# Performance work log

Measured on AMD Instinct MI355X. Metric: run time of the kernel, lower is better.

## Reference

```python
import jax, jax.numpy as jnp
import numpy as np

IN_DIM = 512
HID = 1024
E = 16
TOPK = 2


def setup_inputs() -> dict:
    key = jax.random.key(0)
    ks = jax.random.split(key, 8)
    s = 0.02
    x = jax.random.normal(ks[0], (4, 2048, IN_DIM), dtype=jnp.float32)
    Wr = jax.random.normal(ks[1], (IN_DIM, E), dtype=jnp.float32) * s
    br = jnp.zeros((E,), dtype=jnp.float32)
    W1 = jax.random.normal(ks[2], (E, IN_DIM, HID), dtype=jnp.float32) * s
    b1 = jnp.zeros((E, HID), dtype=jnp.float32)
    W2 = jax.random.normal(ks[3], (E, HID, IN_DIM), dtype=jnp.float32) * s
    b2 = jnp.zeros((E, IN_DIM), dtype=jnp.float32)
    return {"x": x, "Wr": Wr, "br": br, "W1": W1, "b1": b1, "W2": W2, "b2": b2}


def reference(x, Wr, br, W1, b1, W2, b2):
    token_shape = x.shape[:-1]
    xf = x.reshape(-1, x.shape[-1])            # [T, D]
    T = xf.shape[0]

    # router (temperature = 1.0)
    logits = xf @ Wr + br                       # [T, E]
    probs = jax.nn.softmax(logits, axis=-1)
    topk_w, topk_idx = jax.lax.top_k(probs, TOPK)           # [T, K]
    topk_w = topk_w / jnp.maximum(topk_w.sum(-1, keepdims=True), 1e-9)

    # combine weights: [T, E], zero where not routed
    combine = jnp.zeros((T, E), dtype=xf.dtype).at[
        jnp.arange(T)[:, None], topk_idx].add(topk_w)

    # per-expert MLP (exact GELU, as torch nn.GELU default), weighted combine
    y = jnp.zeros_like(xf)
    for e in range(E):
        h = jax.nn.gelu(xf @ W1[e] + b1[e], approximate=False)  # [T, H]
        o = h @ W2[e] + b2[e]                                   # [T, D]
        y = y + combine[:, e:e + 1] * o

    # residual (in_dim == out_dim)
    y = xf + y
    return y.reshape(*token_shape, IN_DIM)
```

## Files before the change

kernel.cpp:

```cpp
#include <hip/hip_runtime.h>
#include <hip/hip_bf16.h>
#include <math.h>

#define IN_DIM 512
#define HID    1024
#define NE     16
#define T_TOK  8192
#define NPAIR  (T_TOK*2)

typedef __attribute__((ext_vector_type(8))) short bf16x8;
typedef __attribute__((ext_vector_type(4))) float f32x4;

__device__ __forceinline__ unsigned short f2b(float f){
  unsigned u = __float_as_uint(f);
  u += 0x7FFF + ((u >> 16) & 1);
  return (unsigned short)(u >> 16);
}
__device__ __forceinline__ float b2f(unsigned short u){
  return __uint_as_float(((unsigned)u) << 16);
}

__device__ __forceinline__ void barrier_lds_only(){
  asm volatile("s_waitcnt lgkmcnt(0)" ::: "memory");
  __builtin_amdgcn_s_barrier();
}

__global__ __launch_bounds__(256) void tconv_kernel(const float* __restrict__ in,
                                                    unsigned short* __restrict__ out,
                                                    int M, int N){
  __shared__ float tile[32][33];
  int e  = blockIdx.z;
  int m0 = blockIdx.y*32, n0 = blockIdx.x*32;
  const float* src = in + (size_t)e*M*N;
  unsigned short* dst = out + (size_t)e*M*N;
  int c = threadIdx.x & 31, r = threadIdx.x >> 5;
  #pragma unroll
  for (int i=0;i<4;i++)
    tile[r + i*8][c] = src[(size_t)(m0 + r + i*8)*N + n0 + c];
  __syncthreads();
  int tr  = threadIdx.x >> 3;
  int tc4 = (threadIdx.x & 7) * 4;
  ushort4 o;
  o.x = f2b(tile[tc4+0][tr]); o.y = f2b(tile[tc4+1][tr]);
  o.z = f2b(tile[tc4+2][tr]); o.w = f2b(tile[tc4+3][tr]);
  *(ushort4*)(&dst[(size_t)(n0 + tr)*M + m0 + tc4]) = o;
}

__global__ __launch_bounds__(256) void router_kernel(
    const float* __restrict__ x, const float* __restrict__ Wr, const float* __restrict__ br,
    unsigned short* __restrict__ xb, int* __restrict__ eid, float* __restrict__ pw)
{
  int wid = threadIdx.x >> 6, lane = threadIdx.x & 63;
  int t = blockIdx.x*4 + wid;
  const float4* xr4 = (const float4*)(x + (size_t)t*IN_DIM);
  ushort4*      xb4 = (ushort4*)(xb + (size_t)t*IN_DIM);

  float acc[NE];
  #pragma unroll
  for (int i=0;i<NE;i++) acc[i]=0.f;

  #pragma unroll
  for (int j=0;j<2;j++){
    int f = j*64 + lane;
    float4 v = xr4[f];
    ushort4 o; o.x=f2b(v.x); o.y=f2b(v.y); o.z=f2b(v.z); o.w=f2b(v.w);
    xb4[f] = o;
    const float4* wr4 = (const float4*)(Wr + (size_t)(f*4)*NE);
    const float* vv = (const float*)&v;
    #pragma unroll
    for (int rr=0; rr<4; rr++){
      float xv = vv[rr];
      #pragma unroll
      for (int q=0;q<4;q++){
        float4 w = wr4[rr*4+q];
        acc[q*4+0] += xv*w.x; acc[q*4+1] += xv*w.y;
        acc[q*4+2] += xv*w.z; acc[q*4+3] += xv*w.w;
      }
    }
  }
  #pragma unroll
  for (int off=32; off>=1; off>>=1){
    #pragma unroll
    for (int i=0;i<NE;i++) acc[i] += __shfl_xor(acc[i], off, 64);
  }
  if (lane==0){
    #pragma unroll
    for (int i=0;i<NE;i++) acc[i] += br[i];
    int e0=0; float l0=acc[0];
    #pragma unroll
    for (int i=1;i<NE;i++) if (acc[i] > l0){ l0=acc[i]; e0=i; }
    int e1=-1; float l1=-3.0e38f;
    #pragma unroll
    for (int i=0;i<NE;i++) if (i!=e0 && acc[i] > l1){ l1=acc[i]; e1=i; }
    float w0 = 1.f/(1.f + __expf(l1 - l0));
    float w1 = 1.f - w0;
    pw[t*2+0] = w0; pw[t*2+1] = w1;
    eid[t*2+0] = e0; eid[t*2+1] = e1;
  }
}

__global__ __launch_bounds__(1024) void bucket_kernel(const int* __restrict__ eid,
                                                      int* __restrict__ cnt,
                                                      int* __restrict__ bucket){
  int e = blockIdx.x;
  __shared__ int lbase;
  if (threadIdx.x == 0) lbase = 0;
  __syncthreads();
  int lane = threadIdx.x & 63, wid = threadIdx.x >> 6;
  int* be = bucket + e*T_TOK;
  for (int c = wid*64; c < NPAIR; c += 1024){
    int p = c + lane;
    bool ok = (eid[p] == e);
    unsigned long long m = __ballot(ok);
    int rank = __popcll(m & ((1ull << lane) - 1ull));
    int count = __popcll(m);
    int base = 0;
    if (lane == 0) base = atomicAdd(&lbase, count);
    base = __shfl(base, 0, 64);
    if (ok) be[base + rank] = p;
  }
  __syncthreads();
  if (threadIdx.x == 0) cnt[e] = lbase;
}

template<int KDIM, int NDIM, bool FIRST>
__global__ __launch_bounds__(256) void moe_gemm(
    const unsigned short* __restrict__ A,
    const unsigned short* __restrict__ Bm,
    const float* __restrict__ bias,
    const int* __restrict__ cnt,
    const int* __restrict__ bucket,
    const float* __restrict__ pw,
    unsigned short* __restrict__ hb,
    unsigned short* __restrict__ opb)
{
  int e  = blockIdx.z;
  int n0 = blockIdx.x * 128;
  int i0 = blockIdx.y * 64;
  int ce = cnt[e];
  if (i0 >= ce) return;
  constexpr int NS = KDIM / 32;

  __shared__ unsigned short As[2*64*32];
  __shared__ unsigned short Bs[2*128*32];

  int tid = threadIdx.x;
  int lane = tid & 63, wid = tid >> 6;
  int wm = (wid>>1)*32, wn = (wid&1)*64;

  int lr0 = tid >> 2;
  int c   = tid & 3;
  int sc  = (c ^ ((lr0 >> 1) & 3)) * 8;
  int wA  = lr0*32 + sc;
  const int* buck = bucket + e*T_TOK;
  int posA  = i0 + lr0;
  int pairA = (posA < ce) ? buck[posA] : buck[i0];
  const unsigned short* Ag = A + (size_t)(FIRST ? (pairA >> 1) : pairA) * KDIM + c*8;
  const unsigned short* Bg = Bm + (size_t)e*NDIM*KDIM + (size_t)(n0 + lr0)*KDIM + c*8;

  f32x4 acc[2][4];
  #pragma unroll
  for (int a=0;a<2;a++)
    #pragma unroll
    for (int b=0;b<4;b++)
      #pragma unroll
      for (int j=0;j<4;j++) acc[a][b][j] = 0.f;

  int fr = lane & 15, fb = lane >> 4;
  int pf8 = (fb ^ ((fr >> 1) & 3)) * 8;

  float4 ar, br0, br1;
  ar  = *(const float4*)(Ag);
  br0 = *(const float4*)(Bg);
  br1 = *(const float4*)(Bg + (size_t)64*KDIM);
  *(float4*)(As + wA) = ar;
  *(float4*)(Bs + wA) = br0;
  *(float4*)(Bs + wA + 64*32) = br1;
  ar  = *(const float4*)(Ag + 32);
  br0 = *(const float4*)(Bg + 32);
  br1 = *(const float4*)(Bg + (size_t)64*KDIM + 32);
  barrier_lds_only();

  #pragma unroll 2
  for (int k = 0; k < NS; k++){
    const int cur = k & 1, nxt = cur ^ 1;
    float4 na, nb0, nb1;
    bool ld = (k + 2 < NS);
    if (ld){
      na  = *(const float4*)(Ag + (k+2)*32);
      nb0 = *(const float4*)(Bg + (k+2)*32);
      nb1 = *(const float4*)(Bg + (size_t)64*KDIM + (k+2)*32);
    }
    if (k + 1 < NS){
      *(float4*)(As + nxt*2048 + wA) = ar;
      *(float4*)(Bs + nxt*4096 + wA) = br0;
      *(float4*)(Bs + nxt*4096 + wA + 64*32) = br1;
    }
    if (ld){ ar = na; br0 = nb0; br1 = nb1; }

    const unsigned short* Ac = As + cur*2048;
    const unsigned short* Bc = Bs + cur*4096;
    bf16x8 af[2], bfr[4];
    #pragma unroll
    for (int s=0;s<2;s++) af[s]  = *(const bf16x8*)(Ac + (wm + s*16 + fr)*32 + pf8);
    #pragma unroll
    for (int u=0;u<4;u++) bfr[u] = *(const bf16x8*)(Bc + (wn + u*16 + fr)*32 + pf8);
    #pragma unroll
    for (int s=0;s<2;s++)
      #pragma unroll
      for (int u=0;u<4;u++)
        acc[s][u] = __builtin_amdgcn_mfma_f32_16x16x32_bf16(af[s], bfr[u], acc[s][u], 0,0,0);
    barrier_lds_only();
  }

  int fq = (lane>>4)*4;
  #pragma unroll
  for (int s=0;s<2;s++){
    #pragma unroll
    for (int i=0;i<4;i++){
      int row = wm + s*16 + fq + i;
      int pos = i0 + row;
      if (pos >= ce) continue;
      int pair = buck[pos];
      float w = FIRST ? 0.f : pw[pair];
      #pragma unroll
      for (int u=0;u<4;u++){
        int n = n0 + wn + u*16 + fr;
        float v = acc[s][u][i] + bias[e*NDIM + n];
        if (FIRST){
          float g = 0.5f*v*(1.f + erff(v*0.70710678118654752f));
          hb[(size_t)pair*NDIM + n] = f2b(g);
        } else {
          opb[(size_t)pair*NDIM + n] = f2b(w*v);
        }
      }
    }
  }
}

__global__ __launch_bounds__(256) void combine_kernel(const float* __restrict__ x,
                                                      const unsigned short* __restrict__ opb,
                                                      float* __restrict__ out){
  int i = blockIdx.x*256 + threadIdx.x;
  int t  = i >> 7;
  int c4 = i & 127;
  float4 v = ((const float4*)x)[i];
  ushort4 a = ((const ushort4*)opb)[(size_t)(2*t)*128 + c4];
  ushort4 b = ((const ushort4*)opb)[(size_t)(2*t+1)*128 + c4];
  v.x += b2f(a.x) + b2f(b.x);
  v.y += b2f(a.y) + b2f(b.y);
  v.z += b2f(a.z) + b2f(b.z);
  v.w += b2f(a.w) + b2f(b.w);
  ((float4*)out)[i] = v;
}

extern "C" void kernel_launch(void* const* d_in, const int* in_sizes, int n_in,
                              void* d_out, int out_size, void* d_ws, size_t ws_size,
                              hipStream_t stream)
{
  const float* x  = (const float*)d_in[0];
  const float* Wr = (const float*)d_in[1];
  const float* br = (const float*)d_in[2];
  const float* W1 = (const float*)d_in[3];
  const float* b1 = (const float*)d_in[4];
  const float* W2 = (const float*)d_in[5];
  const float* b2 = (const float*)d_in[6];
  float* out = (float*)d_out;
  char* ws = (char*)d_ws;

  int*            cnt    = (int*)(ws + 0);
  int*            bucket = (int*)(ws + 1024);
  float*          pw     = (float*)(ws + 525312);
  unsigned short* xb     = (unsigned short*)(ws + 590848);
  unsigned short* w1t    = (unsigned short*)(ws + 8979456);
  unsigned short* w2t    = (unsigned short*)(ws + 25756672);
  unsigned short* hb     = (unsigned short*)(ws + 42533888);
  int*            eid    = (int*)(ws + 42533888);
  unsigned short* opb    = w1t;

  router_kernel<<<T_TOK/4, 256, 0, stream>>>(x, Wr, br, xb, eid, pw);
  bucket_kernel<<<NE, 1024, 0, stream>>>(eid, cnt, bucket);
  tconv_kernel<<<dim3(HID/32, IN_DIM/32, NE), 256, 0, stream>>>(W1, w1t, IN_DIM, HID);
  tconv_kernel<<<dim3(IN_DIM/32, HID/32, NE), 256, 0, stream>>>(W2, w2t, HID, IN_DIM);
  moe_gemm<IN_DIM, HID, true ><<<dim3(HID/128,    T_TOK/64, NE), 256, 0, stream>>>(
      xb, w1t, b1, cnt, bucket, pw, hb, opb);
  moe_gemm<HID, IN_DIM, false><<<dim3(IN_DIM/128, T_TOK/64, NE), 256, 0, stream>>>(
      hb, w2t, b2, cnt, bucket, pw, hb, opb);
  combine_kernel<<<(T_TOK*IN_DIM/4)/256, 256, 0, stream>>>(x, opb, out);
}
```

Measured before the change: 286.9 us.

## Store hidden activations expert-contiguous and deepen global prefetch to three stages

The first GEMM now writes GELU outputs into an expert-sorted contiguous buffer indexed by a per-expert prefix offset, instead of scattering them by pair index. The second GEMM can then read its A rows contiguously rather than gathering through the bucket list. The k-loop also keeps two register prefetch stages in flight instead of one. The cost is a serial prefix-sum loop over expert counts in every block and more registers held live.

```diff
diff --git a/kernel.cpp b/kernel.cpp
--- a/kernel.cpp
+++ b/kernel.cpp
@@ -139,6 +139,8 @@
   int i0 = blockIdx.y * 64;
   int ce = cnt[e];
   if (i0 >= ce) return;
+  int ebase = 0;
+  for (int j=0;j<e;j++) ebase += cnt[j];
   constexpr int NS = KDIM / 32;
 
   __shared__ unsigned short As[2*64*32];
@@ -154,8 +156,15 @@
   int wA  = lr0*32 + sc;
   const int* buck = bucket + e*T_TOK;
   int posA  = i0 + lr0;
-  int pairA = (posA < ce) ? buck[posA] : buck[i0];
-  const unsigned short* Ag = A + (size_t)(FIRST ? (pairA >> 1) : pairA) * KDIM + c*8;
+  int arow;
+  if (FIRST){
+    int pair = (posA < ce) ? buck[posA] : buck[i0];
+    arow = pair >> 1;
+  } else {
+    arow = ebase + posA;
+    if (arow > NPAIR-1) arow = NPAIR-1;
+  }
+  const unsigned short* Ag = A + (size_t)arow*KDIM + c*8;
   const unsigned short* Bg = Bm + (size_t)e*NDIM*KDIM + (size_t)(n0 + lr0)*KDIM + c*8;
 
   f32x4 acc[2][4];
@@ -169,47 +178,53 @@
   int fr = lane & 15, fb = lane >> 4;
   int pf8 = (fb ^ ((fr >> 1) & 3)) * 8;
 
-  float4 ar, br0, br1;
-  ar  = *(const float4*)(Ag);
-  br0 = *(const float4*)(Bg);
-  br1 = *(const float4*)(Bg + (size_t)64*KDIM);
-  *(float4*)(As + wA) = ar;
-  *(float4*)(Bs + wA) = br0;
-  *(float4*)(Bs + wA + 64*32) = br1;
-  ar  = *(const float4*)(Ag + 32);
-  br0 = *(const float4*)(Bg + 32);
-  br1 = *(const float4*)(Bg + (size_t)64*KDIM + 32);
-  barrier_lds_only();
+  {
+    float4 a0 = *(const float4*)(Ag);
+    float4 b0 = *(const float4*)(Bg);
+    float4 b1 = *(const float4*)(Bg + (size_t)64*KDIM);
+    *(float4*)(As + wA) = a0;
+    *(float4*)(Bs + wA) = b0;
+    *(float4*)(Bs + wA + 64*32) = b1;
+  }
+  float4 pa[2], pb0[2], pb1[2];
+  #pragma unroll
+  for (int s=0;s<2;s++){
+    int kk = (s+1)*32;
+    bool ok = (s+1) < NS;
+    if (ok){
+      pa[s]  = *(const float4*)(Ag + kk);
+      pb0[s] = *(const float4*)(Bg + kk);
+      pb1[s] = *(const float4*)(Bg + (size_t)64*KDIM + kk);
+    }
+  }
+  __syncthreads();
 
   #pragma unroll 2
   for (int k = 0; k < NS; k++){
-    const int cur = k & 1, nxt = cur ^ 1;
-    float4 na, nb0, nb1;
-    bool ld = (k + 2 < NS);
-    if (ld){
-      na  = *(const float4*)(Ag + (k+2)*32);
-      nb0 = *(const float4*)(Bg + (k+2)*32);
-      nb1 = *(const float4*)(Bg + (size_t)64*KDIM + (k+2)*32);
-    }
+    const int cur = k & 1, nxt = cur ^ 1, s = k & 1;
     if (k + 1 < NS){
-      *(float4*)(As + nxt*2048 + wA) = ar;
-      *(float4*)(Bs + nxt*4096 + wA) = br0;
-      *(float4*)(Bs + nxt*4096 + wA + 64*32) = br1;
-    }
-    if (ld){ ar = na; br0 = nb0; br1 = nb1; }
-
+      *(float4*)(As + nxt*2048 + wA) = pa[s];
+      *(float4*)(Bs + nxt*4096 + wA) = pb0[s];
+      *(float4*)(Bs + nxt*4096 + wA + 64*32) = pb1[s];
+    }
+    if (k + 3 < NS){
+      int kk = (k+3)*32;
+      pa[s]  = *(const float4*)(Ag + kk);
+      pb0[s] = *(const float4*)(Bg + kk);
+      pb1[s] = *(const float4*)(Bg + (size_t)64*KDIM + kk);
+    }
     const unsigned short* Ac = As + cur*2048;
     const unsigned short* Bc = Bs + cur*4096;
     bf16x8 af[2], bfr[4];
     #pragma unroll
-    for (int s=0;s<2;s++) af[s]  = *(const bf16x8*)(Ac + (wm + s*16 + fr)*32 + pf8);
-    #pragma unroll
-    for (int u=0;u<4;u++) bfr[u] = *(const bf16x8*)(Bc + (wn + u*16 + fr)*32 + pf8);
-    #pragma unroll
-    for (int s=0;s<2;s++)
+    for (int s2=0;s2<2;s2++) af[s2]  = *(const bf16x8*)(Ac + (wm + s2*16 + fr)*32 + pf8);
+    #pragma unroll
+    for (int u=0;u<4;u++)    bfr[u]  = *(const bf16x8*)(Bc + (wn + u*16 + fr)*32 + pf8);
+    #pragma unroll
+    for (int s2=0;s2<2;s2++)
       #pragma unroll
       for (int u=0;u<4;u++)
-        acc[s][u] = __builtin_amdgcn_mfma_f32_16x16x32_bf16(af[s], bfr[u], acc[s][u], 0,0,0);
+        acc[s2][u] = __builtin_amdgcn_mfma_f32_16x16x32_bf16(af[s2], bfr[u], acc[s2][u], 0,0,0);
     barrier_lds_only();
   }
 
@@ -221,17 +236,16 @@
       int row = wm + s*16 + fq + i;
       int pos = i0 + row;
       if (pos >= ce) continue;
-      int pair = buck[pos];
-      float w = FIRST ? 0.f : pw[pair];
       #pragma unroll
       for (int u=0;u<4;u++){
         int n = n0 + wn + u*16 + fr;
         float v = acc[s][u][i] + bias[e*NDIM + n];
         if (FIRST){
           float g = 0.5f*v*(1.f + erff(v*0.70710678118654752f));
-          hb[(size_t)pair*NDIM + n] = f2b(g);
+          hb[(size_t)(ebase + pos)*NDIM + n] = f2b(g);
         } else {
-          opb[(size_t)pair*NDIM + n] = f2b(w*v);
+          int pair = buck[pos];
+          opb[(size_t)pair*NDIM + n] = f2b(pw[pair]*v);
         }
       }
     }
```

After: 464.9 us. +62.0%, slower.

## Use persistent tile scheduler over routed expert tiles and compact hidden layout

Applied to the files above, without the earlier changes.

Replaces the dense 3D grid (most blocks exit early because each expert holds only a fraction of tokens) with a fixed 1024-block persistent grid that loops over only the valid tiles, computed by a prefix scan of expert counts. The hidden activations are now stored contiguously per expert (ebase + pos) instead of at pair positions, so the second GEMM reads A rows sequentially without a gather. This removes launch and early-exit overhead for empty tiles and improves locality, at the cost of recomputing the tile-to-expert mapping inside each block and a fixed grid size.

```diff
diff --git a/kernel.cpp b/kernel.cpp
--- a/kernel.cpp
+++ b/kernel.cpp
@@ -134,12 +134,12 @@
     unsigned short* __restrict__ hb,
     unsigned short* __restrict__ opb)
 {
-  int e  = blockIdx.z;
-  int n0 = blockIdx.x * 128;
-  int i0 = blockIdx.y * 64;
-  int ce = cnt[e];
-  if (i0 >= ce) return;
-  constexpr int NS = KDIM / 32;
+  constexpr int NS  = KDIM / 32;
+  constexpr int NBT = NDIM / 128;
+
+  int ntiles = 0;
+  #pragma unroll
+  for (int j=0;j<NE;j++) ntiles += ((cnt[j]+63)>>6)*NBT;
 
   __shared__ unsigned short As[2*64*32];
   __shared__ unsigned short Bs[2*128*32];
@@ -147,91 +147,114 @@
   int tid = threadIdx.x;
   int lane = tid & 63, wid = tid >> 6;
   int wm = (wid>>1)*32, wn = (wid&1)*64;
-
   int lr0 = tid >> 2;
   int c   = tid & 3;
   int sc  = (c ^ ((lr0 >> 1) & 3)) * 8;
   int wA  = lr0*32 + sc;
-  const int* buck = bucket + e*T_TOK;
-  int posA  = i0 + lr0;
-  int pairA = (posA < ce) ? buck[posA] : buck[i0];
-  const unsigned short* Ag = A + (size_t)(FIRST ? (pairA >> 1) : pairA) * KDIM + c*8;
-  const unsigned short* Bg = Bm + (size_t)e*NDIM*KDIM + (size_t)(n0 + lr0)*KDIM + c*8;
-
-  f32x4 acc[2][4];
-  #pragma unroll
-  for (int a=0;a<2;a++)
-    #pragma unroll
-    for (int b=0;b<4;b++)
-      #pragma unroll
-      for (int j=0;j<4;j++) acc[a][b][j] = 0.f;
-
   int fr = lane & 15, fb = lane >> 4;
   int pf8 = (fb ^ ((fr >> 1) & 3)) * 8;
-
-  float4 ar, br0, br1;
-  ar  = *(const float4*)(Ag);
-  br0 = *(const float4*)(Bg);
-  br1 = *(const float4*)(Bg + (size_t)64*KDIM);
-  *(float4*)(As + wA) = ar;
-  *(float4*)(Bs + wA) = br0;
-  *(float4*)(Bs + wA + 64*32) = br1;
-  ar  = *(const float4*)(Ag + 32);
-  br0 = *(const float4*)(Bg + 32);
-  br1 = *(const float4*)(Bg + (size_t)64*KDIM + 32);
-  barrier_lds_only();
-
-  #pragma unroll 2
-  for (int k = 0; k < NS; k++){
-    const int cur = k & 1, nxt = cur ^ 1;
-    float4 na, nb0, nb1;
-    bool ld = (k + 2 < NS);
-    if (ld){
-      na  = *(const float4*)(Ag + (k+2)*32);
-      nb0 = *(const float4*)(Bg + (k+2)*32);
-      nb1 = *(const float4*)(Bg + (size_t)64*KDIM + (k+2)*32);
-    }
-    if (k + 1 < NS){
-      *(float4*)(As + nxt*2048 + wA) = ar;
-      *(float4*)(Bs + nxt*4096 + wA) = br0;
-      *(float4*)(Bs + nxt*4096 + wA + 64*32) = br1;
-    }
-    if (ld){ ar = na; br0 = nb0; br1 = nb1; }
-
-    const unsigned short* Ac = As + cur*2048;
-    const unsigned short* Bc = Bs + cur*4096;
-    bf16x8 af[2], bfr[4];
-    #pragma unroll
-    for (int s=0;s<2;s++) af[s]  = *(const bf16x8*)(Ac + (wm + s*16 + fr)*32 + pf8);
-    #pragma unroll
-    for (int u=0;u<4;u++) bfr[u] = *(const bf16x8*)(Bc + (wn + u*16 + fr)*32 + pf8);
-    #pragma unroll
-    for (int s=0;s<2;s++)
-      #pragma unroll
-      for (int u=0;u<4;u++)
-        acc[s][u] = __builtin_amdgcn_mfma_f32_16x16x32_bf16(af[s], bfr[u], acc[s][u], 0,0,0);
+  int fq = (lane>>4)*4;
+
+  for (int t = blockIdx.x; t < ntiles; t += gridDim.x){
+    int e=0, tloc=0, ebase=0, ce=0, itl=1;
+    {
+      int cum=0, crow=0;
+      #pragma unroll
+      for (int j=0;j<NE;j++){
+        int cj = cnt[j];
+        int it = (cj+63)>>6;
+        int tj = it * NBT;
+        bool in = (t >= cum) & (t < cum+tj);
+        if (in){ e=j; tloc=t-cum; ebase=crow; ce=cj; itl=it; }
+        cum += tj; crow += cj;
+      }
+    }
+    int i0 = (tloc % itl) * 64;
+    int n0 = (tloc / itl) * 128;
+
+    const int* buck = bucket + e*T_TOK;
+    int posA = i0 + lr0;
+    int arow;
+    if (FIRST){
+      int pair = (posA < ce) ? buck[posA] : buck[i0];
+      arow = pair >> 1;
+    } else {
+      arow = ebase + posA;
+      if (arow > NPAIR-1) arow = NPAIR-1;
+    }
+    const unsigned short* Ag = A + (size_t)arow*KDIM + c*8;
+    const unsigned short* Bg = Bm + (size_t)e*NDIM*KDIM + (size_t)(n0 + lr0)*KDIM + c*8;
+
+    f32x4 acc[2][4];
+    #pragma unroll
+    for (int a=0;a<2;a++)
+      #pragma unroll
+      for (int b=0;b<4;b++)
+        #pragma unroll
+        for (int j=0;j<4;j++) acc[a][b][j] = 0.f;
+
+    float4 ar, br0, br1;
+    ar  = *(const float4*)(Ag);
+    br0 = *(const float4*)(Bg);
+    br1 = *(const float4*)(Bg + (size_t)64*KDIM);
+    *(float4*)(As + wA) = ar;
+    *(float4*)(Bs + wA) = br0;
+    *(float4*)(Bs + wA + 64*32) = br1;
+    ar  = *(const float4*)(Ag + 32);
+    br0 = *(const float4*)(Bg + 32);
+    br1 = *(const float4*)(Bg + (size_t)64*KDIM + 32);
     barrier_lds_only();
-  }
-
-  int fq = (lane>>4)*4;
-  #pragma unroll
-  for (int s=0;s<2;s++){
-    #pragma unroll
-    for (int i=0;i<4;i++){
-      int row = wm + s*16 + fq + i;
-      int pos = i0 + row;
-      if (pos >= ce) continue;
-      int pair = buck[pos];
-      float w = FIRST ? 0.f : pw[pair];
-      #pragma unroll
-      for (int u=0;u<4;u++){
-        int n = n0 + wn + u*16 + fr;
-        float v = acc[s][u][i] + bias[e*NDIM + n];
-        if (FIRST){
-          float g = 0.5f*v*(1.f + erff(v*0.70710678118654752f));
-          hb[(size_t)pair*NDIM + n] = f2b(g);
-        } else {
-          opb[(size_t)pair*NDIM + n] = f2b(w*v);
+
+    #pragma unroll 2
+    for (int k = 0; k < NS; k++){
+      const int cur = k & 1, nxt = cur ^ 1;
+      float4 na, nb0, nb1;
+      bool ld = (k + 2 < NS);
+      if (ld){
+        na  = *(const float4*)(Ag + (k+2)*32);
+        nb0 = *(const float4*)(Bg + (k+2)*32);
+        nb1 = *(const float4*)(Bg + (size_t)64*KDIM + (k+2)*32);
+      }
+      if (k + 1 < NS){
+        *(float4*)(As + nxt*2048 + wA) = ar;
+        *(float4*)(Bs + nxt*4096 + wA) = br0;
+        *(float4*)(Bs + nxt*4096 + wA + 64*32) = br1;
+      }
+      if (ld){ ar = na; br0 = nb0; br1 = nb1; }
+
+      const unsigned short* Ac = As + cur*2048;
+      const unsigned short* Bc = Bs + cur*4096;
+      bf16x8 af[2], bfr[4];
+      #pragma unroll
+      for (int s=0;s<2;s++) af[s]  = *(const bf16x8*)(Ac + (wm + s*16 + fr)*32 + pf8);
+      #pragma unroll
+      for (int u=0;u<4;u++) bfr[u] = *(const bf16x8*)(Bc + (wn + u*16 + fr)*32 + pf8);
+      #pragma unroll
+      for (int s=0;s<2;s++)
+        #pragma unroll
+        for (int u=0;u<4;u++)
+          acc[s][u] = __builtin_amdgcn_mfma_f32_16x16x32_bf16(af[s], bfr[u], acc[s][u], 0,0,0);
+      barrier_lds_only();
+    }
+
+    #pragma unroll
+    for (int s=0;s<2;s++){
+      #pragma unroll
+      for (int i=0;i<4;i++){
+        int row = wm + s*16 + fq + i;
+        int pos = i0 + row;
+        if (pos >= ce) continue;
+        #pragma unroll
+        for (int u=0;u<4;u++){
+          int n = n0 + wn + u*16 + fr;
+          float v = acc[s][u][i] + bias[e*NDIM + n];
+          if (FIRST){
+            float g = 0.5f*v*(1.f + erff(v*0.70710678118654752f));
+            hb[(size_t)(ebase + pos)*NDIM + n] = f2b(g);
+          } else {
+            int pair = buck[pos];
+            opb[(size_t)pair*NDIM + n] = f2b(pw[pair]*v);
+          }
         }
       }
     }
@@ -282,9 +305,9 @@
   bucket_kernel<<<NE, 1024, 0, stream>>>(eid, cnt, bucket);
   tconv_kernel<<<dim3(HID/32, IN_DIM/32, NE), 256, 0, stream>>>(W1, w1t, IN_DIM, HID);
   tconv_kernel<<<dim3(IN_DIM/32, HID/32, NE), 256, 0, stream>>>(W2, w2t, HID, IN_DIM);
-  moe_gemm<IN_DIM, HID, true ><<<dim3(HID/128,    T_TOK/64, NE), 256, 0, stream>>>(
+  moe_gemm<IN_DIM, HID, true ><<<1024, 256, 0, stream>>>(
       xb, w1t, b1, cnt, bucket, pw, hb, opb);
-  moe_gemm<HID, IN_DIM, false><<<dim3(IN_DIM/128, T_TOK/64, NE), 256, 0, stream>>>(
+  moe_gemm<HID, IN_DIM, false><<<1024, 256, 0, stream>>>(
       hb, w2t, b2, cnt, bucket, pw, hb, opb);
   combine_kernel<<<(T_TOK*IN_DIM/4)/256, 256, 0, stream>>>(x, opb, out);
 }
```

Result: no change. 282.9 us (-1.4%).
